# Kernel tuning notes

Measured on AMD Instinct MI355X. Metric: run time of the kernel, lower is better.

## Reference

```python
import jax, jax.numpy as jnp
import numpy as np

D_MODEL = 512
NUM_HEADS = 8
D_HEAD = D_MODEL // NUM_HEADS


def setup_inputs() -> dict:
    key = jax.random.key(0)
    kx, kq, kk, kv, ko = jax.random.split(key, 5)
    s = 1.0 / np.sqrt(D_MODEL)
    return {
        "X": jax.random.normal(kx, (2, 4096, D_MODEL), dtype=jnp.float32),
        "Wq": jax.random.normal(kq, (D_MODEL, D_MODEL), dtype=jnp.float32) * s,
        "Wk": jax.random.normal(kk, (D_MODEL, D_MODEL), dtype=jnp.float32) * s,
        "Wv": jax.random.normal(kv, (D_MODEL, D_MODEL), dtype=jnp.float32) * s,
        "Wo": jax.random.normal(ko, (D_MODEL, D_MODEL), dtype=jnp.float32) * s,
    }


def reference(X, Wq, Wk, Wv, Wo):
    B, L, D = X.shape
    H, dh = NUM_HEADS, D_HEAD
    # Linear projections (torch Linear: y = x @ W.T), split heads -> [B, H, L, dh]
    def proj(W):
        return (X @ W.T).reshape(B, L, H, dh).transpose(0, 2, 1, 3)
    Q, K, V = proj(Wq), proj(Wk), proj(Wv)
    # Scaled dot-product attention; scores [B, H, L, L]
    scores = jnp.einsum("bhqd,bhkd->bhqk", Q, K) / jnp.sqrt(jnp.asarray(dh, X.dtype))
    attn = jax.nn.softmax(scores, axis=-1)
    out = jnp.einsum("bhqk,bhkd->bhqd", attn, V)  # [B, H, L, dh]
    out = out.transpose(0, 2, 1, 3).reshape(B, L, D)
    return out @ Wo.T
```

## Files before the change

### kernel.cpp

```cpp
#include <hip/hip_runtime.h>
#include <math.h>

#define D_MODEL 512
#define NHEADS  8
#define DH      64
#define LSEQ    4096
#define NB      2
#define M_TOT   (NB * LSEQ)

typedef __attribute__((ext_vector_type(8))) short bf16x8;
typedef __attribute__((ext_vector_type(4))) float f32x4;
typedef __attribute__((ext_vector_type(8))) unsigned short ushort8v;

#define MFMA16(a, b, c) __builtin_amdgcn_mfma_f32_16x16x32_bf16(a, b, c, 0, 0, 0)

__device__ __forceinline__ ushort f2bf(float x) {
    unsigned u = __builtin_bit_cast(unsigned, x);
    u += 0x7fffu + ((u >> 16) & 1u);
    return (ushort)(u >> 16);
}

__device__ __forceinline__ unsigned cvt_pk_bf16(float a, float b) {
    unsigned r;
    asm("v_cvt_pk_bf16_f32 %0, %1, %2" : "=v"(r) : "v"(a), "v"(b));
    return r;
}

__device__ __forceinline__ float fexp2(float x) {
#if __has_builtin(__builtin_amdgcn_exp2f)
    return __builtin_amdgcn_exp2f(x);
#else
    return exp2f(x);
#endif
}

__device__ __forceinline__ void gload16(const void* g, void* l) {
    __builtin_amdgcn_global_load_lds(
        (const __attribute__((address_space(1))) unsigned*)g,
        (__attribute__((address_space(3))) unsigned*)l, 16, 0, 0);
}

__global__ __launch_bounds__(256) void cast_all(
    const float* __restrict__ X,  const float* __restrict__ Wq,
    const float* __restrict__ Wk, const float* __restrict__ Wv,
    const float* __restrict__ Wo,
    ushort* __restrict__ Xb,  ushort* __restrict__ Wqb,
    ushort* __restrict__ Wkb, ushort* __restrict__ Wvb,
    ushort* __restrict__ Wob)
{
    const int seg = blockIdx.y;
    const float* src = seg == 0 ? X : seg == 1 ? Wq : seg == 2 ? Wk
                      : seg == 3 ? Wv : Wo;
    ushort* dst = seg == 0 ? Xb : seg == 1 ? Wqb : seg == 2 ? Wkb
                 : seg == 3 ? Wvb : Wob;
    const int n = (seg == 0) ? M_TOT * D_MODEL : D_MODEL * D_MODEL;
    const int idx = (blockIdx.x * 256 + threadIdx.x) * 8;
    if (idx >= n) return;
    float4 a = *(const float4*)(src + idx);
    float4 b = *(const float4*)(src + idx + 4);
    ushort8v o;
    o[0] = f2bf(a.x); o[1] = f2bf(a.y); o[2] = f2bf(a.z); o[3] = f2bf(a.w);
    o[4] = f2bf(b.x); o[5] = f2bf(b.y); o[6] = f2bf(b.z); o[7] = f2bf(b.w);
    *(ushort8v*)(dst + idx) = o;
}

__device__ __forceinline__ void gemm_core(
    const ushort* __restrict__ A, const ushort* __restrict__ Bw,
    ushort (*Alds)[64], ushort (*Blds)[64], f32x4 acc[4][4],
    int m0, int n0, int w, int lg, int lr)
{
    const int tid = threadIdx.x;
    const int wr = w >> 1, wc = w & 1;
    const int srow = tid >> 3;
    const int scol = (tid & 7) * 8;

    for (int k0 = 0; k0 < D_MODEL; k0 += 64) {
        __syncthreads();
        #pragma unroll
        for (int i = 0; i < 4; ++i) {
            gload16(A  + (size_t)(m0 + i * 32 + srow) * D_MODEL + k0 + scol,
                    (char*)Alds + i * 4096 + w * 1024);
            gload16(Bw + (size_t)(n0 + i * 32 + srow) * D_MODEL + k0 + scol,
                    (char*)Blds + i * 4096 + w * 1024);
        }
        __syncthreads();
        #pragma unroll
        for (int kk = 0; kk < 2; ++kk) {
            bf16x8 af[4], bfr[4];
            #pragma unroll
            for (int i = 0; i < 4; ++i)
                af[i] = *(const bf16x8*)&Alds[wr * 64 + 16 * i + lr][kk * 32 + 8 * lg];
            #pragma unroll
            for (int j = 0; j < 4; ++j)
                bfr[j] = *(const bf16x8*)&Blds[wc * 64 + 16 * j + lr][kk * 32 + 8 * lg];
            #pragma unroll
            for (int i = 0; i < 4; ++i)
                #pragma unroll
                for (int j = 0; j < 4; ++j)
                    acc[i][j] = MFMA16(af[i], bfr[j], acc[i][j]);
        }
    }
}

__global__ __launch_bounds__(256) void gemm_qkv(
    const ushort* __restrict__ Xb,
    const ushort* __restrict__ Wqb, const ushort* __restrict__ Wkb,
    const ushort* __restrict__ Wvb,
    ushort* __restrict__ Qb, ushort* __restrict__ Kb, ushort* __restrict__ Vtb)
{
    __shared__ __align__(16) ushort Alds[128][64];
    __shared__ __align__(16) ushort Blds[128][64];

    const int mode = blockIdx.z;
    const ushort* Bw = mode == 0 ? Wqb : mode == 1 ? Wkb : Wvb;

    const int tid = threadIdx.x;
    const int w = tid >> 6, l = tid & 63;
    const int lg = l >> 4, lr = l & 15;
    const int wr = w >> 1, wc = w & 1;
    const int m0 = blockIdx.x * 128;
    const int n0 = blockIdx.y * 128;

    f32x4 acc[4][4];
    #pragma unroll
    for (int i = 0; i < 4; ++i)
        #pragma unroll
        for (int j = 0; j < 4; ++j) acc[i][j] = (f32x4){0.f, 0.f, 0.f, 0.f};

    gemm_core(Xb, Bw, Alds, Blds, acc, m0, n0, w, lg, lr);

    if (mode < 2) {
        const float scale = (mode == 0) ? 0.125f * 1.44269504088896f : 1.0f;
        ushort* Yb = (mode == 0) ? Qb : Kb;
        #pragma unroll
        for (int i = 0; i < 4; ++i) {
            const int mb = m0 + wr * 64 + 16 * i + 4 * lg;
            const int b = mb >> 12, lq = mb & 4095;
            #pragma unroll
            for (int j = 0; j < 4; ++j) {
                const int ng = n0 + wc * 64 + 16 * j + lr;
                const int h = ng >> 6, dh = ng & 63;
                ushort* Yp = Yb + ((size_t)(b * NHEADS + h) * LSEQ + lq) * DH + dh;
                #pragma unroll
                for (int r = 0; r < 4; ++r)
                    Yp[(size_t)r * DH] = f2bf(acc[i][j][r] * scale);
            }
        }
    } else {
        #pragma unroll
        for (int i = 0; i < 4; ++i) {
            const int mb = m0 + wr * 64 + 16 * i + 4 * lg;
            const int b = mb >> 12, lq = mb & 4095;
            #pragma unroll
            for (int j = 0; j < 4; ++j) {
                const int ng = n0 + wc * 64 + 16 * j + lr;
                const int h = ng >> 6, dh = ng & 63;
                ushort4 w4;
                w4.x = f2bf(acc[i][j][0]); w4.y = f2bf(acc[i][j][1]);
                w4.z = f2bf(acc[i][j][2]); w4.w = f2bf(acc[i][j][3]);
                *(ushort4*)(Vtb + ((size_t)(b * NHEADS + h) * DH + dh) * LSEQ + lq) = w4;
            }
        }
    }
}

__global__ __launch_bounds__(256) void gemm_wo(
    const ushort* __restrict__ Cb, const ushort* __restrict__ Wob,
    float* __restrict__ out)
{
    __shared__ __align__(16) ushort Alds[128][64];
    __shared__ __align__(16) ushort Blds[128][64];

    const int tid = threadIdx.x;
    const int w = tid >> 6, l = tid & 63;
    const int lg = l >> 4, lr = l & 15;
    const int wr = w >> 1, wc = w & 1;
    const int m0 = blockIdx.x * 128;
    const int n0 = blockIdx.y * 128;

    f32x4 acc[4][4];
    #pragma unroll
    for (int i = 0; i < 4; ++i)
        #pragma unroll
        for (int j = 0; j < 4; ++j) acc[i][j] = (f32x4){0.f, 0.f, 0.f, 0.f};

    gemm_core(Cb, Wob, Alds, Blds, acc, m0, n0, w, lg, lr);

    #pragma unroll
    for (int i = 0; i < 4; ++i) {
        const int mb = m0 + wr * 64 + 16 * i + 4 * lg;
        #pragma unroll
        for (int j = 0; j < 4; ++j) {
            const int ng = n0 + wc * 64 + 16 * j + lr;
            float* Yp = out + (size_t)mb * D_MODEL + ng;
            #pragma unroll
            for (int r = 0; r < 4; ++r)
                Yp[(size_t)r * D_MODEL] = acc[i][j][r];
        }
    }
}

#define QBLK 128
#define KBLK 64

__global__ __launch_bounds__(256) void flash_mfma(
    const ushort* __restrict__ Q, const ushort* __restrict__ K,
    const ushort* __restrict__ Vt, ushort* __restrict__ Cb)
{
    __shared__ __align__(16) ushort Klds[64][72];
    __shared__ __align__(16) ushort Vlds[64][72];
    __shared__ __align__(16) ushort Plds[128][72];

    const int tid = threadIdx.x;
    const int w  = tid >> 6;
    const int l  = tid & 63;
    const int lg = l >> 4;
    const int lr = l & 15;

    const int bh = blockIdx.y;
    const int q0 = blockIdx.x * QBLK;

    bf16x8 qa[2][2];
    #pragma unroll
    for (int u = 0; u < 2; ++u) {
        const ushort* qp = Q + ((size_t)bh * LSEQ + q0 + 32 * w + 16 * u + lr) * DH + 8 * lg;
        qa[u][0] = *(const bf16x8*)(qp);
        qa[u][1] = *(const bf16x8*)(qp + 32);
    }

    float lsum[2] = {0.f, 0.f};
    f32x4 o4[2][4];
    #pragma unroll
    for (int u = 0; u < 2; ++u)
        #pragma unroll
        for (int ot = 0; ot < 4; ++ot) o4[u][ot] = (f32x4){0.f, 0.f, 0.f, 0.f};

    const int srow = tid >> 2;
    const int scol = (tid & 3) << 4;
    const ushort* Kp = K  + (size_t)bh * LSEQ * DH;
    const ushort* Vp = Vt + (size_t)bh * DH * LSEQ;

    uint4 kA, kB, vA, vB;
    {
        const ushort* ks = Kp + (size_t)srow * DH + scol;
        const ushort* vs = Vp + (size_t)srow * LSEQ + scol;
        kA = *(const uint4*)(ks); kB = *(const uint4*)(ks + 8);
        vA = *(const uint4*)(vs); vB = *(const uint4*)(vs + 8);
    }

    for (int kt = 0; kt < LSEQ; kt += KBLK) {
        __syncthreads();
        *(uint4*)&Klds[srow][scol] = kA;  *(uint4*)&Klds[srow][scol + 8] = kB;
        *(uint4*)&Vlds[srow][scol] = vA;  *(uint4*)&Vlds[srow][scol + 8] = vB;
        __syncthreads();

        if (kt + KBLK < LSEQ) {
            const ushort* ks = Kp + (size_t)(kt + KBLK + srow) * DH + scol;
            const ushort* vs = Vp + (size_t)srow * LSEQ + (kt + KBLK) + scol;
            kA = *(const uint4*)(ks); kB = *(const uint4*)(ks + 8);
            vA = *(const uint4*)(vs); vB = *(const uint4*)(vs + 8);
        }

        f32x4 s[2][4];
        #pragma unroll
        for (int kt2 = 0; kt2 < 4; ++kt2) {
            bf16x8 k0 = *(const bf16x8*)&Klds[kt2 * 16 + lr][8 * lg];
            bf16x8 k1 = *(const bf16x8*)&Klds[kt2 * 16 + lr][32 + 8 * lg];
            f32x4 z = (f32x4){0.f, 0.f, 0.f, 0.f};
            s[0][kt2] = MFMA16(k1, qa[0][1], MFMA16(k0, qa[0][0], z));
            s[1][kt2] = MFMA16(k1, qa[1][1], MFMA16(k0, qa[1][0], z));
        }

        #pragma unroll
        for (int u = 0; u < 2; ++u) {
            float rs = 0.f;
            #pragma unroll
            for (int kt2 = 0; kt2 < 4; ++kt2) {
                const float p0 = fexp2(s[u][kt2][0]);
                const float p1 = fexp2(s[u][kt2][1]);
                const float p2 = fexp2(s[u][kt2][2]);
                const float p3 = fexp2(s[u][kt2][3]);
                rs += (p0 + p1) + (p2 + p3);
                uint2 pw;
                pw.x = cvt_pk_bf16(p0, p1);
                pw.y = cvt_pk_bf16(p2, p3);
                *(uint2*)&Plds[32 * w + 16 * u + lr][kt2 * 16 + 4 * lg] = pw;
            }
            lsum[u] += rs;
        }

        #pragma unroll
        for (int vh = 0; vh < 2; ++vh) {
            bf16x8 p0 = *(const bf16x8*)&Plds[32 * w + lr][32 * vh + 8 * lg];
            bf16x8 p1 = *(const bf16x8*)&Plds[32 * w + 16 + lr][32 * vh + 8 * lg];
            #pragma unroll
            for (int ot = 0; ot < 4; ++ot) {
                bf16x8 vv = *(const bf16x8*)&Vlds[16 * ot + lr][32 * vh + 8 * lg];
                o4[0][ot] = MFMA16(p0, vv, o4[0][ot]);
                o4[1][ot] = MFMA16(p1, vv, o4[1][ot]);
            }
        }
    }

    const int b = bh >> 3, h = bh & 7;
    #pragma unroll
    for (int u = 0; u < 2; ++u) {
        float t = lsum[u];
        t += __shfl_xor(t, 16);
        t += __shfl_xor(t, 32);
        const float inv = 1.0f / t;
        #pragma unroll
        for (int r = 0; r < 4; ++r) {
            const float ivr = __shfl(inv, 4 * lg + r);
            const int qrow = q0 + 32 * w + 16 * u + 4 * lg + r;
            ushort* op = Cb + ((size_t)b * LSEQ + qrow) * D_MODEL + h * DH + lr;
            #pragma unroll
            for (int ot = 0; ot < 4; ++ot)
                op[16 * ot] = f2bf(o4[u][ot][r] * ivr);
        }
    }
}

extern "C" void kernel_launch(void* const* d_in, const int* in_sizes, int n_in,
                              void* d_out, int out_size, void* d_ws, size_t ws_size,
                              hipStream_t stream)
{
    const float* X  = (const float*)d_in[0];
    const float* Wq = (const float*)d_in[1];
    const float* Wk = (const float*)d_in[2];
    const float* Wv = (const float*)d_in[3];
    const float* Wo = (const float*)d_in[4];
    float* out = (float*)d_out;

    char* ws = (char*)d_ws;
    const size_t szX = (size_t)M_TOT * D_MODEL * 2;
    const size_t szW = (size_t)D_MODEL * D_MODEL * 2;
    ushort* Xb  = (ushort*)(ws);
    ushort* Wqb = (ushort*)(ws + szX);
    ushort* Wkb = (ushort*)(ws + szX + szW);
    ushort* Wvb = (ushort*)(ws + szX + 2 * szW);
    ushort* Wob = (ushort*)(ws + szX + 3 * szW);
    ushort* Qb  = (ushort*)(ws + szX + 4 * szW);
    ushort* Kb  = (ushort*)(ws + 2 * szX + 4 * szW);
    ushort* Vtb = (ushort*)(ws + 3 * szX + 4 * szW);
    ushort* Cbb = (ushort*)(ws + 4 * szX + 4 * szW);

    dim3 gc(M_TOT * D_MODEL / (256 * 8), 5);
    cast_all<<<gc, 256, 0, stream>>>(X, Wq, Wk, Wv, Wo, Xb, Wqb, Wkb, Wvb, Wob);

    dim3 gq(M_TOT / 128, D_MODEL / 128, 3);
    gemm_qkv<<<gq, 256, 0, stream>>>(Xb, Wqb, Wkb, Wvb, Qb, Kb, Vtb);

    dim3 gf(LSEQ / QBLK, NB * NHEADS);
    flash_mfma<<<gf, 256, 0, stream>>>(Qb, Kb, Vtb, Cbb);

    dim3 go(M_TOT / 128, D_MODEL / 128);
    gemm_wo<<<go, 256, 0, stream>>>(Cbb, Wob, out);
}
```

Baseline: 148.9 us.

## Split attention over two key halves and combine partial outputs

```diff
diff --git a/kernel.cpp b/kernel.cpp
--- a/kernel.cpp
+++ b/kernel.cpp
@@ -7,6 +7,8 @@
 #define LSEQ    4096
 #define NB      2
 #define M_TOT   (NB * LSEQ)
+#define NSPLIT  2
+#define KHALF   (LSEQ / NSPLIT)
 
 typedef __attribute__((ext_vector_type(8))) short bf16x8;
 typedef __attribute__((ext_vector_type(4))) float f32x4;
@@ -18,6 +20,11 @@
     unsigned u = __builtin_bit_cast(unsigned, x);
     u += 0x7fffu + ((u >> 16) & 1u);
     return (ushort)(u >> 16);
+}
+
+__device__ __forceinline__ float bf2f(ushort u) {
+    unsigned v = ((unsigned)u) << 16;
+    return __builtin_bit_cast(float, v);
 }
 
 __device__ __forceinline__ unsigned cvt_pk_bf16(float a, float b) {
@@ -205,11 +212,12 @@
 
 __global__ __launch_bounds__(256) void flash_mfma(
     const ushort* __restrict__ Q, const ushort* __restrict__ K,
-    const ushort* __restrict__ Vt, ushort* __restrict__ Cb)
-{
-    __shared__ __align__(16) ushort Klds[64][72];
-    __shared__ __align__(16) ushort Vlds[64][72];
-    __shared__ __align__(16) ushort Plds[128][72];
+    const ushort* __restrict__ Vt, ushort* __restrict__ Op,
+    float* __restrict__ Ls)
+{
+    __shared__ __align__(16) ushort Klds[64][68];
+    __shared__ __align__(16) ushort Vlds[64][68];
+    __shared__ __align__(16) ushort Plds[128][68];
 
     const int tid = threadIdx.x;
     const int w  = tid >> 6;
@@ -219,6 +227,9 @@
 
     const int bh = blockIdx.y;
     const int q0 = blockIdx.x * QBLK;
+    const int z  = blockIdx.z;
+    const int kt0  = z * KHALF;
+    const int kend = kt0 + KHALF;
 
     bf16x8 qa[2][2];
     #pragma unroll
@@ -242,19 +253,19 @@
 
     uint4 kA, kB, vA, vB;
     {
-        const ushort* ks = Kp + (size_t)srow * DH + scol;
-        const ushort* vs = Vp + (size_t)srow * LSEQ + scol;
+        const ushort* ks = Kp + (size_t)(kt0 + srow) * DH + scol;
+        const ushort* vs = Vp + (size_t)srow * LSEQ + kt0 + scol;
         kA = *(const uint4*)(ks); kB = *(const uint4*)(ks + 8);
         vA = *(const uint4*)(vs); vB = *(const uint4*)(vs + 8);
     }
 
-    for (int kt = 0; kt < LSEQ; kt += KBLK) {
+    for (int kt = kt0; kt < kend; kt += KBLK) {
         __syncthreads();
         *(uint4*)&Klds[srow][scol] = kA;  *(uint4*)&Klds[srow][scol + 8] = kB;
         *(uint4*)&Vlds[srow][scol] = vA;  *(uint4*)&Vlds[srow][scol + 8] = vB;
         __syncthreads();
 
-        if (kt + KBLK < LSEQ) {
+        if (kt + KBLK < kend) {
             const ushort* ks = Kp + (size_t)(kt + KBLK + srow) * DH + scol;
             const ushort* vs = Vp + (size_t)srow * LSEQ + (kt + KBLK) + scol;
             kA = *(const uint4*)(ks); kB = *(const uint4*)(ks + 8);
@@ -266,9 +277,9 @@
         for (int kt2 = 0; kt2 < 4; ++kt2) {
             bf16x8 k0 = *(const bf16x8*)&Klds[kt2 * 16 + lr][8 * lg];
             bf16x8 k1 = *(const bf16x8*)&Klds[kt2 * 16 + lr][32 + 8 * lg];
-            f32x4 z = (f32x4){0.f, 0.f, 0.f, 0.f};
-            s[0][kt2] = MFMA16(k1, qa[0][1], MFMA16(k0, qa[0][0], z));
-            s[1][kt2] = MFMA16(k1, qa[1][1], MFMA16(k0, qa[1][0], z));
+            f32x4 z4 = (f32x4){0.f, 0.f, 0.f, 0.f};
+            s[0][kt2] = MFMA16(k1, qa[0][1], MFMA16(k0, qa[0][0], z4));
+            s[1][kt2] = MFMA16(k1, qa[1][1], MFMA16(k0, qa[1][0], z4));
         }
 
         #pragma unroll
@@ -303,22 +314,48 @@
     }
 
     const int b = bh >> 3, h = bh & 7;
+    ushort* Opz = Op + (size_t)z * M_TOT * D_MODEL;
     #pragma unroll
     for (int u = 0; u < 2; ++u) {
         float t = lsum[u];
         t += __shfl_xor(t, 16);
         t += __shfl_xor(t, 32);
-        const float inv = 1.0f / t;
+        if (lg == 0)
+            Ls[((size_t)z * NB * NHEADS + bh) * LSEQ + q0 + 32 * w + 16 * u + lr] = t;
         #pragma unroll
         for (int r = 0; r < 4; ++r) {
-            const float ivr = __shfl(inv, 4 * lg + r);
             const int qrow = q0 + 32 * w + 16 * u + 4 * lg + r;
-            ushort* op = Cb + ((size_t)b * LSEQ + qrow) * D_MODEL + h * DH + lr;
+            ushort* op = Opz + ((size_t)b * LSEQ + qrow) * D_MODEL + h * DH + lr;
             #pragma unroll
             for (int ot = 0; ot < 4; ++ot)
-                op[16 * ot] = f2bf(o4[u][ot][r] * ivr);
-        }
-    }
+                op[16 * ot] = f2bf(o4[u][ot][r]);
+        }
+    }
+}
+
+__global__ __launch_bounds__(256) void combine(
+    const ushort* __restrict__ Op, const float* __restrict__ Ls,
+    ushort* __restrict__ Cb)
+{
+    const int idx = blockIdx.x * 256 + threadIdx.x;
+    const int row = idx >> 6;
+    const int col0 = (idx & 63) << 3;
+    const int b = row >> 12, lq = row & 4095;
+    const int h = col0 >> 6;
+    const int bh = b * NHEADS + h;
+
+    const float l0 = Ls[(size_t)bh * LSEQ + lq];
+    const float l1 = Ls[((size_t)NB * NHEADS + bh) * LSEQ + lq];
+    const float inv = 1.0f / (l0 + l1);
+
+    const size_t off = (size_t)row * D_MODEL + col0;
+    ushort8v a0 = *(const ushort8v*)(Op + off);
+    ushort8v a1 = *(const ushort8v*)(Op + (size_t)M_TOT * D_MODEL + off);
+    ushort8v o;
+    #pragma unroll
+    for (int i = 0; i < 8; ++i)
+        o[i] = f2bf((bf2f(a0[i]) + bf2f(a1[i])) * inv);
+    *(ushort8v*)(Cb + off) = o;
 }
 
 extern "C" void kernel_launch(void* const* d_in, const int* in_sizes, int n_in,
@@ -343,7 +380,9 @@
     ushort* Qb  = (ushort*)(ws + szX + 4 * szW);
     ushort* Kb  = (ushort*)(ws + 2 * szX + 4 * szW);
     ushort* Vtb = (ushort*)(ws + 3 * szX + 4 * szW);
-    ushort* Cbb = (ushort*)(ws + 4 * szX + 4 * szW);
+    ushort* Opb = (ushort*)(ws + 4 * szX + 4 * szW);
+    float*  Lsb = (float*) (ws + 6 * szX + 4 * szW);
+    ushort* Cbb = (ushort*)(ws + 6 * szX + 4 * szW + (size_t)NSPLIT * NB * NHEADS * LSEQ * 4);
 
     dim3 gc(M_TOT * D_MODEL / (256 * 8), 5);
     cast_all<<<gc, 256, 0, stream>>>(X, Wq, Wk, Wv, Wo, Xb, Wqb, Wkb, Wvb, Wob);
@@ -351,8 +390,11 @@
     dim3 gq(M_TOT / 128, D_MODEL / 128, 3);
     gemm_qkv<<<gq, 256, 0, stream>>>(Xb, Wqb, Wkb, Wvb, Qb, Kb, Vtb);
 
-    dim3 gf(LSEQ / QBLK, NB * NHEADS);
-    flash_mfma<<<gf, 256, 0, stream>>>(Qb, Kb, Vtb, Cbb);
+    dim3 gf(LSEQ / QBLK, NB * NHEADS, NSPLIT);
+    flash_mfma<<<gf, 256, 0, stream>>>(Qb, Kb, Vtb, Opb, Lsb);
+
+    dim3 gm(M_TOT * D_MODEL / (256 * 8));
+    combine<<<gm, 256, 0, stream>>>(Opb, Lsb, Cbb);
 
     dim3 go(M_TOT / 128, D_MODEL / 128);
     gemm_wo<<<go, 256, 0, stream>>>(Cbb, Wob, out);
```

Measured after the change: 153.8 us. +3.3%, slower.
